# Kernel optimization log

Measured on AMD Instinct MI355X. Metric: run time of the kernel, lower is better.

## Reference

```python
import jax, jax.numpy as jnp
import numpy as np

H = 64  # hidden_size hardcoded in the module


def setup_inputs() -> dict:
    key = jax.random.key(0)
    ks = jax.random.split(key, 8)
    B, T, I, O = 4096, 256, 128, 10
    s_ih = 1.0 / np.sqrt(H)
    return {
        "x": jax.random.normal(ks[0], (B, T, I), dtype=jnp.float32),
        # PyTorch LSTM params, gate order (i, f, g, o)
        "W_ih": jax.random.uniform(ks[1], (4 * H, I), minval=-s_ih, maxval=s_ih, dtype=jnp.float32),
        "W_hh": jax.random.uniform(ks[2], (4 * H, H), minval=-s_ih, maxval=s_ih, dtype=jnp.float32),
        "b_ih": jax.random.uniform(ks[3], (4 * H,), minval=-s_ih, maxval=s_ih, dtype=jnp.float32),
        "b_hh": jax.random.uniform(ks[4], (4 * H,), minval=-s_ih, maxval=s_ih, dtype=jnp.float32),
        "W_out": jax.random.uniform(ks[5], (O, H), minval=-s_ih, maxval=s_ih, dtype=jnp.float32),
        "b_out": jax.random.uniform(ks[6], (O,), minval=-s_ih, maxval=s_ih, dtype=jnp.float32),
    }


def _lstm_last_h(x, W_ih, W_hh, b_ih, b_hh):
    B, T, I = x.shape
    # Precompute input contributions for all timesteps: [T, B, 4H]
    gx = jnp.einsum('bti,gi->tbg', x, W_ih) + (b_ih + b_hh)

    def step(carry, g_t):
        h, c = carry
        g = g_t + h @ W_hh.T  # [B, 4H]
        i = jax.nn.sigmoid(g[:, 0 * H:1 * H])
        f = jax.nn.sigmoid(g[:, 1 * H:2 * H])
        gg = jnp.tanh(g[:, 2 * H:3 * H])
        o = jax.nn.sigmoid(g[:, 3 * H:4 * H])
        c = f * c + i * gg
        h = o * jnp.tanh(c)
        return (h, c), None

    h0 = jnp.zeros((B, H), dtype=x.dtype)
    c0 = jnp.zeros((B, H), dtype=x.dtype)
    (h_last, _), _ = jax.lax.scan(step, (h0, c0), gx)
    return h_last


def reference(x, W_ih, W_hh, b_ih, b_hh, W_out, b_out):
    # forward reshapes x to [B, T, I]; our x is already that shape.
    h_last = _lstm_last_h(x, W_ih, W_hh, b_ih, b_hh)  # r_out[:, -1, :]
    return h_last @ W_out.T + b_out
```

## Files before the change

kernel.cpp:

```cpp
#include <hip/hip_runtime.h>


typedef __attribute__((ext_vector_type(8))) short bf16x8;
typedef __attribute__((ext_vector_type(4))) float f32x4;
typedef __attribute__((ext_vector_type(4))) int i32x4;

#define T_STEPS 256
#define L2E 1.44269504f

__device__ __forceinline__ short f2bf(float f) {
    unsigned u = __float_as_uint(f);
    u += 0x7FFFu + ((u >> 16) & 1u);
    return (short)(u >> 16);
}
__device__ __forceinline__ unsigned cvt_pk(float lo, float hi) {
    unsigned r;
    asm("v_cvt_pk_bf16_f32 %0, %1, %2" : "=v"(r) : "v"(lo), "v"(hi));
    return r;
}
__device__ __forceinline__ float frcp(float x) {
    float r; asm("v_rcp_f32 %0, %1" : "=v"(r) : "v"(x)); return r;
}
__device__ __forceinline__ float fexp2(float x) {
    float r; asm("v_exp_f32 %0, %1" : "=v"(r) : "v"(x)); return r;
}
__device__ __forceinline__ float sigm(float x) { return frcp(1.0f + fexp2(x * -L2E)); }
__device__ __forceinline__ float tanh_f(float x) { return 1.0f - 2.0f * frcp(1.0f + fexp2(x * (2.0f * L2E))); }

#define MF(A, Bf, C) (C) = __builtin_amdgcn_mfma_f32_16x16x32_bf16((A), (Bf), (C), 0, 0, 0)
#define PACK8(Av, Bv, W) { (W).x = cvt_pk((Av)[0], (Av)[1]); (W).y = cvt_pk((Av)[2], (Av)[3]); \
                           (W).z = cvt_pk((Bv)[0], (Bv)[1]); (W).w = cvt_pk((Bv)[2], (Bv)[3]); }

__global__ __launch_bounds__(256, 1) void lstm_fused_kernel(
    const float* __restrict__ x,
    const float* __restrict__ W_ih,
    const float* __restrict__ W_hh,
    const float* __restrict__ b_ih,
    const float* __restrict__ b_hh,
    const float* __restrict__ W_out,
    const float* __restrict__ b_out,
    float* __restrict__ out)
{
    __shared__ __align__(16) char smem[24576];

    const int tid  = threadIdx.x;
    const int lane = tid & 63;
    const int q    = tid >> 6;
    const int l15  = lane & 15;
    const int l4   = lane >> 4;
    const int b0   = blockIdx.x * 16;

    bf16x8 Bih[4][4];
    bf16x8 Bhh[4][2];
    f32x4  biasC[4];
#pragma unroll
    for (int nt = 0; nt < 4; ++nt) {
        const int row = nt * 64 + q * 16 + l15;
#pragma unroll
        for (int ks = 0; ks < 4; ++ks) {
            const float* p = W_ih + row * 128 + ks * 32 + l4 * 8;
            f32x4 a = *(const f32x4*)p;
            f32x4 b = *(const f32x4*)(p + 4);
            bf16x8 w;
#pragma unroll
            for (int j = 0; j < 4; ++j) { w[j] = f2bf(a[j]); w[4 + j] = f2bf(b[j]); }
            Bih[nt][ks] = w;
        }
#pragma unroll
        for (int ks = 0; ks < 2; ++ks) {
            const float* p = W_hh + row * 64 + ks * 32 + l4 * 8;
            f32x4 a = *(const f32x4*)p;
            f32x4 b = *(const f32x4*)(p + 4);
            bf16x8 w;
#pragma unroll
            for (int j = 0; j < 4; ++j) { w[j] = f2bf(a[j]); w[4 + j] = f2bf(b[j]); }
            Bhh[nt][ks] = w;
        }
        const float bb = b_ih[row] + b_hh[row];
        biasC[nt] = (f32x4){bb, bb, bb, bb};
    }

    const int sc  = tid & 15;
    const int sb  = tid >> 4;
    const int sks = sc >> 2;
    const int schunk = ((sc & 3) << 4) | sb;
    const int xf_wr  = (((sks * 64 + schunk) * 16) ^ ((sks & 3) << 6));
    const float* xrow = x + (size_t)(b0 + sb) * T_STEPS * 128 + sc * 8;

    int xf_rd[4];
#pragma unroll
    for (int ks = 0; ks < 4; ++ks)
        xf_rd[ks] = (((ks * 64 + lane) * 16) ^ ((ks & 3) << 6));

    int hb_wr[4];
#pragma unroll
    for (int r = 0; r < 4; ++r) {
        const int b = l4 * 4 + r;
        const int j = q * 16 + l15;
        hb_wr[r] = ((b * 128 + j * 2) ^ ((b & 7) << 4) ^ ((b >> 3) << 5));
    }
    int hb_rd[2];
#pragma unroll
    for (int ks = 0; ks < 2; ++ks)
        hb_rd[ks] = ((l15 * 128 + ks * 64 + l4 * 16) ^ ((l15 & 7) << 4) ^ ((l15 >> 3) << 5));

#pragma unroll
    for (int s = 0; s < 3; ++s) {
        f32x4 a = *(const f32x4*)(xrow + (size_t)s * 128);
        f32x4 b = *(const f32x4*)(xrow + (size_t)s * 128 + 4);
        i32x4 w; PACK8(a, b, w);
        *(i32x4*)(smem + s * 4096 + xf_wr) = w;
    }
    f32x4 P0_[4], P1_[4];
#pragma unroll
    for (int s = 0; s < 4; ++s) {
        P0_[s] = *(const f32x4*)(xrow + (size_t)(s + 3) * 128);
        P1_[s] = *(const f32x4*)(xrow + (size_t)(s + 3) * 128 + 4);
    }
    ((unsigned long long*)(smem + 16384 + 2048))[tid] = 0ull;

    asm volatile("s_waitcnt lgkmcnt(0)" ::: "memory");
    __builtin_amdgcn_s_barrier();

    float c[4]  = {0.f, 0.f, 0.f, 0.f};
    float hl[4] = {0.f, 0.f, 0.f, 0.f};

    f32x4 accA[4], accB[4];
    {
        bf16x8 Ax0 = *(const bf16x8*)(smem + xf_rd[0]);
        bf16x8 Ax1 = *(const bf16x8*)(smem + xf_rd[1]);
        bf16x8 Ax2 = *(const bf16x8*)(smem + xf_rd[2]);
        bf16x8 Ax3 = *(const bf16x8*)(smem + xf_rd[3]);
#pragma unroll
        for (int nt = 0; nt < 4; ++nt) accA[nt] = biasC[nt];
        MF(Ax0, Bih[0][0], accA[0]); MF(Ax0, Bih[1][0], accA[1]);
        MF(Ax0, Bih[2][0], accA[2]); MF(Ax0, Bih[3][0], accA[3]);
        MF(Ax1, Bih[0][1], accA[0]); MF(Ax1, Bih[1][1], accA[1]);
        MF(Ax1, Bih[2][1], accA[2]); MF(Ax1, Bih[3][1], accA[3]);
        MF(Ax2, Bih[0][2], accA[0]); MF(Ax2, Bih[1][2], accA[1]);
        MF(Ax2, Bih[2][2], accA[2]); MF(Ax2, Bih[3][2], accA[3]);
        MF(Ax3, Bih[0][3], accA[0]); MF(Ax3, Bih[1][3], accA[1]);
        MF(Ax3, Bih[2][3], accA[2]); MF(Ax3, Bih[3][3], accA[3]);
    }

#define WINDOW(tt, T4, ACUR, ANXT)                                             \
  {                                                                            \
    const char* hbR = smem + 16384 + ((((T4) & 1) ^ 1) * 2048);                \
    char*       hbW = smem + 16384 + (((T4) & 1) * 2048);                      \
    const char* xfb = smem + ((((T4) + 1) & 3) * 4096);                        \
    char*       xfw = smem + ((((T4) + 3) & 3) * 4096);                        \
    bf16x8 Ah0 = *(const bf16x8*)(hbR + hb_rd[0]);                             \
    bf16x8 Ah1 = *(const bf16x8*)(hbR + hb_rd[1]);                             \
    MF(Ah0, Bhh[0][0], ACUR[0]); MF(Ah0, Bhh[1][0], ACUR[1]);                  \
    MF(Ah0, Bhh[2][0], ACUR[2]); MF(Ah0, Bhh[3][0], ACUR[3]);                  \
    MF(Ah1, Bhh[0][1], ACUR[0]); MF(Ah1, Bhh[1][1], ACUR[1]);                  \
    MF(Ah1, Bhh[2][1], ACUR[2]); MF(Ah1, Bhh[3][1], ACUR[3]);                  \
    bf16x8 Ax0 = *(const bf16x8*)(xfb + xf_rd[0]);                             \
    bf16x8 Ax1 = *(const bf16x8*)(xfb + xf_rd[1]);                             \
    bf16x8 Ax2 = *(const bf16x8*)(xfb + xf_rd[2]);                             \
    bf16x8 Ax3 = *(const bf16x8*)(xfb + xf_rd[3]);                             \
    ANXT[0] = biasC[0]; ANXT[1] = biasC[1];                                    \
    ANXT[2] = biasC[2]; ANXT[3] = biasC[3];                                    \
    MF(Ax0, Bih[0][0], ANXT[0]); MF(Ax0, Bih[1][0], ANXT[1]);                  \
    MF(Ax0, Bih[2][0], ANXT[2]); MF(Ax0, Bih[3][0], ANXT[3]);                  \
    MF(Ax1, Bih[0][1], ANXT[0]); MF(Ax1, Bih[1][1], ANXT[1]);                  \
    MF(Ax1, Bih[2][1], ANXT[2]); MF(Ax1, Bih[3][1], ANXT[3]);                  \
    MF(Ax2, Bih[0][2], ANXT[0]); MF(Ax2, Bih[1][2], ANXT[1]);                  \
    MF(Ax2, Bih[2][2], ANXT[2]); MF(Ax2, Bih[3][2], ANXT[3]);                  \
    MF(Ax3, Bih[0][3], ANXT[0]); MF(Ax3, Bih[1][3], ANXT[1]);                  \
    MF(Ax3, Bih[2][3], ANXT[2]); MF(Ax3, Bih[3][3], ANXT[3]);                  \
    {                                                                          \
      i32x4 w; PACK8(P0_[(T4)], P1_[(T4)], w);                                 \
      *(i32x4*)(xfw + xf_wr) = w;                                              \
      int tc = (tt) + 7; tc = tc > 255 ? 255 : tc;                             \
      P0_[(T4)] = *(const f32x4*)(xrow + (size_t)tc * 128);                    \
      P1_[(T4)] = *(const f32x4*)(xrow + (size_t)tc * 128 + 4);                \
    }                                                                          \
    _Pragma("unroll")                                                          \
    for (int r = 0; r < 4; ++r) {                                              \
      float iv = sigm(ACUR[0][r]);                                             \
      float fv = sigm(ACUR[1][r]);                                             \
      float gv = tanh_f(ACUR[2][r]);                                           \
      float ov = sigm(ACUR[3][r]);                                             \
      float cc = fv * c[r] + iv * gv;                                          \
      c[r] = cc;                                                               \
      hl[r] = ov * tanh_f(cc);                                                 \
    }                                                                          \
    {                                                                          \
      unsigned w01 = cvt_pk(hl[0], hl[1]);                                     \
      unsigned w23 = cvt_pk(hl[2], hl[3]);                                     \
      *(short*)(hbW + hb_wr[0]) = (short)w01;                                  \
      *(short*)(hbW + hb_wr[1]) = (short)(w01 >> 16);                          \
      *(short*)(hbW + hb_wr[2]) = (short)w23;                                  \
      *(short*)(hbW + hb_wr[3]) = (short)(w23 >> 16);                          \
    }                                                                          \
    asm volatile("s_waitcnt lgkmcnt(0)" ::: "memory");                         \
    __builtin_amdgcn_s_barrier();                                              \
  }

    for (int t = 0; t < T_STEPS; t += 4) {
        WINDOW(t,     0, accA, accB);
        WINDOW(t + 1, 1, accB, accA);
        WINDOW(t + 2, 2, accA, accB);
        WINDOW(t + 3, 3, accB, accA);
    }
#undef WINDOW

#pragma unroll
    for (int r = 0; r < 4; ++r) {
        const int b = l4 * 4 + r;
        const int j = q * 16 + l15;
        *(float*)(smem + 20480 + (b * 64 + j) * 4) = hl[r];
    }
    asm volatile("s_waitcnt lgkmcnt(0)" ::: "memory");
    __builtin_amdgcn_s_barrier();

    if (tid < 160) {
        const int b = tid / 10;
        const int o = tid - b * 10;
        const f32x4* hf = (const f32x4*)(smem + 20480 + b * 256);
        const f32x4* wr = (const f32x4*)(W_out + o * 64);
        float s = b_out[o];
#pragma unroll
        for (int j4 = 0; j4 < 16; ++j4) {
            f32x4 h4 = hf[j4];
            f32x4 w4 = wr[j4];
            s += h4[0] * w4[0] + h4[1] * w4[1] + h4[2] * w4[2] + h4[3] * w4[3];
        }
        out[(b0 + b) * 10 + o] = s;
    }
}

extern "C" void kernel_launch(void* const* d_in, const int* in_sizes, int n_in,
                              void* d_out, int out_size, void* d_ws, size_t ws_size,
                              hipStream_t stream) {
    const float* x     = (const float*)d_in[0];
    const float* W_ih  = (const float*)d_in[1];
    const float* W_hh  = (const float*)d_in[2];
    const float* b_ih  = (const float*)d_in[3];
    const float* b_hh  = (const float*)d_in[4];
    const float* W_out = (const float*)d_in[5];
    const float* b_out = (const float*)d_in[6];
    (void)in_sizes; (void)n_in; (void)out_size; (void)d_ws; (void)ws_size;

    lstm_fused_kernel<<<dim3(256), dim3(256), 0, stream>>>(
        x, W_ih, W_hh, b_ih, b_hh, W_out, b_out, (float*)d_out);
}
```

Baseline: 177.8 us.

## Double waves per block, split gate nonlinearity across wave pairs

Raises the block from 256 to 512 threads. Each pair of waves computes the same MFMA gate tile redundantly, and each wave evaluates the nonlinearity for only two of the four rows, halving the serial transcendental work per wave on the recurrent critical path. The x staging is re-split so each thread loads one f32x4 instead of two. The cost is duplicated MFMA work, more register pressure under launch_bounds(512,2), and a barrier spanning twice as many waves.

```diff
diff --git a/kernel.cpp b/kernel.cpp
--- a/kernel.cpp
+++ b/kernel.cpp
@@ -3,10 +3,15 @@
 
 typedef __attribute__((ext_vector_type(8))) short bf16x8;
 typedef __attribute__((ext_vector_type(4))) float f32x4;
-typedef __attribute__((ext_vector_type(4))) int i32x4;
+typedef __attribute__((ext_vector_type(2))) unsigned u32x2;
 
 #define T_STEPS 256
 #define L2E 1.44269504f
+
+#define XF_OFF 0
+#define H_OFF  16384
+#define HF_OFF 20480
+#define LDS_SZ 24576
 
 __device__ __forceinline__ short f2bf(float f) {
     unsigned u = __float_as_uint(f);
@@ -18,20 +23,15 @@
     asm("v_cvt_pk_bf16_f32 %0, %1, %2" : "=v"(r) : "v"(lo), "v"(hi));
     return r;
 }
-__device__ __forceinline__ float frcp(float x) {
-    float r; asm("v_rcp_f32 %0, %1" : "=v"(r) : "v"(x)); return r;
-}
-__device__ __forceinline__ float fexp2(float x) {
-    float r; asm("v_exp_f32 %0, %1" : "=v"(r) : "v"(x)); return r;
-}
+__device__ __forceinline__ float frcp(float x) { float r; asm("v_rcp_f32 %0, %1" : "=v"(r) : "v"(x)); return r; }
+__device__ __forceinline__ float fexp2(float x) { float r; asm("v_exp_f32 %0, %1" : "=v"(r) : "v"(x)); return r; }
 __device__ __forceinline__ float sigm(float x) { return frcp(1.0f + fexp2(x * -L2E)); }
 __device__ __forceinline__ float tanh_f(float x) { return 1.0f - 2.0f * frcp(1.0f + fexp2(x * (2.0f * L2E))); }
 
 #define MF(A, Bf, C) (C) = __builtin_amdgcn_mfma_f32_16x16x32_bf16((A), (Bf), (C), 0, 0, 0)
-#define PACK8(Av, Bv, W) { (W).x = cvt_pk((Av)[0], (Av)[1]); (W).y = cvt_pk((Av)[2], (Av)[3]); \
-                           (W).z = cvt_pk((Bv)[0], (Bv)[1]); (W).w = cvt_pk((Bv)[2], (Bv)[3]); }
-
-__global__ __launch_bounds__(256, 1) void lstm_fused_kernel(
+#define SYNC { asm volatile("s_waitcnt lgkmcnt(0)" ::: "memory"); __builtin_amdgcn_s_barrier(); }
+
+__global__ __launch_bounds__(512, 2) void lstm_kernel(
     const float* __restrict__ x,
     const float* __restrict__ W_ih,
     const float* __restrict__ W_hh,
@@ -41,11 +41,13 @@
     const float* __restrict__ b_out,
     float* __restrict__ out)
 {
-    __shared__ __align__(16) char smem[24576];
+    __shared__ __align__(16) char smem[LDS_SZ];
 
     const int tid  = threadIdx.x;
     const int lane = tid & 63;
-    const int q    = tid >> 6;
+    const int w    = tid >> 6;
+    const int m    = w >> 1;
+    const int e    = w & 1;
     const int l15  = lane & 15;
     const int l4   = lane >> 4;
     const int b0   = blockIdx.x * 16;
@@ -55,82 +57,80 @@
     f32x4  biasC[4];
 #pragma unroll
     for (int nt = 0; nt < 4; ++nt) {
-        const int row = nt * 64 + q * 16 + l15;
+        const int row = nt * 64 + m * 16 + l15;
 #pragma unroll
         for (int ks = 0; ks < 4; ++ks) {
             const float* p = W_ih + row * 128 + ks * 32 + l4 * 8;
             f32x4 a = *(const f32x4*)p;
             f32x4 b = *(const f32x4*)(p + 4);
-            bf16x8 w;
-#pragma unroll
-            for (int j = 0; j < 4; ++j) { w[j] = f2bf(a[j]); w[4 + j] = f2bf(b[j]); }
-            Bih[nt][ks] = w;
+            bf16x8 wv;
+#pragma unroll
+            for (int j = 0; j < 4; ++j) { wv[j] = f2bf(a[j]); wv[4 + j] = f2bf(b[j]); }
+            Bih[nt][ks] = wv;
         }
 #pragma unroll
         for (int ks = 0; ks < 2; ++ks) {
             const float* p = W_hh + row * 64 + ks * 32 + l4 * 8;
             f32x4 a = *(const f32x4*)p;
             f32x4 b = *(const f32x4*)(p + 4);
-            bf16x8 w;
-#pragma unroll
-            for (int j = 0; j < 4; ++j) { w[j] = f2bf(a[j]); w[4 + j] = f2bf(b[j]); }
-            Bhh[nt][ks] = w;
+            bf16x8 wv;
+#pragma unroll
+            for (int j = 0; j < 4; ++j) { wv[j] = f2bf(a[j]); wv[4 + j] = f2bf(b[j]); }
+            Bhh[nt][ks] = wv;
         }
         const float bb = b_ih[row] + b_hh[row];
         biasC[nt] = (f32x4){bb, bb, bb, bb};
     }
 
-    const int sc  = tid & 15;
-    const int sb  = tid >> 4;
-    const int sks = sc >> 2;
-    const int schunk = ((sc & 3) << 4) | sb;
-    const int xf_wr  = (((sks * 64 + schunk) * 16) ^ ((sks & 3) << 6));
-    const float* xrow = x + (size_t)(b0 + sb) * T_STEPS * 128 + sc * 8;
-
     int xf_rd[4];
 #pragma unroll
     for (int ks = 0; ks < 4; ++ks)
         xf_rd[ks] = (((ks * 64 + lane) * 16) ^ ((ks & 3) << 6));
 
-    int hb_wr[4];
-#pragma unroll
-    for (int r = 0; r < 4; ++r) {
-        const int b = l4 * 4 + r;
-        const int j = q * 16 + l15;
-        hb_wr[r] = ((b * 128 + j * 2) ^ ((b & 7) << 4) ^ ((b >> 3) << 5));
+    const int jcol = m * 16 + l15;
+    int hb_wr[2];
+#pragma unroll
+    for (int u = 0; u < 2; ++u) {
+        const int b = l4 * 4 + 2 * e + u;
+        hb_wr[u] = ((b * 128 + jcol * 2) ^ ((b & 7) << 4) ^ ((b >> 3) << 5));
     }
     int hb_rd[2];
 #pragma unroll
     for (int ks = 0; ks < 2; ++ks)
         hb_rd[ks] = ((l15 * 128 + ks * 64 + l4 * 16) ^ ((l15 & 7) << 4) ^ ((l15 >> 3) << 5));
 
+    const int srow = tid >> 5;
+    const int scc  = tid & 31;
+    const int sks  = scc >> 3;
+    const int sl4  = (scc & 7) >> 1;
+    const int sh   = scc & 1;
+    const int xf_wr = (((sks * 64 + sl4 * 16 + srow) * 16 + sh * 8) ^ ((sks & 3) << 6));
+    const float* xsrc = x + (size_t)(b0 + srow) * (T_STEPS * 128) + scc * 4;
+
 #pragma unroll
     for (int s = 0; s < 3; ++s) {
-        f32x4 a = *(const f32x4*)(xrow + (size_t)s * 128);
-        f32x4 b = *(const f32x4*)(xrow + (size_t)s * 128 + 4);
-        i32x4 w; PACK8(a, b, w);
-        *(i32x4*)(smem + s * 4096 + xf_wr) = w;
-    }
-    f32x4 P0_[4], P1_[4];
-#pragma unroll
-    for (int s = 0; s < 4; ++s) {
-        P0_[s] = *(const f32x4*)(xrow + (size_t)(s + 3) * 128);
-        P1_[s] = *(const f32x4*)(xrow + (size_t)(s + 3) * 128 + 4);
-    }
-    ((unsigned long long*)(smem + 16384 + 2048))[tid] = 0ull;
-
-    asm volatile("s_waitcnt lgkmcnt(0)" ::: "memory");
-    __builtin_amdgcn_s_barrier();
-
-    float c[4]  = {0.f, 0.f, 0.f, 0.f};
-    float hl[4] = {0.f, 0.f, 0.f, 0.f};
+        f32x4 v = *(const f32x4*)(xsrc + (size_t)s * 128);
+        u32x2 wv; wv.x = cvt_pk(v[0], v[1]); wv.y = cvt_pk(v[2], v[3]);
+        *(u32x2*)(smem + XF_OFF + s * 4096 + xf_wr) = wv;
+    }
+    f32x4 P[4];
+#pragma unroll
+    for (int s = 0; s < 4; ++s)
+        P[s] = *(const f32x4*)(xsrc + (size_t)(s + 3) * 128);
+
+    ((unsigned*)(smem + H_OFF + 2048))[tid] = 0u;
+
+    SYNC;
+
+    float c[2]  = {0.f, 0.f};
+    float hl[2] = {0.f, 0.f};
 
     f32x4 accA[4], accB[4];
     {
-        bf16x8 Ax0 = *(const bf16x8*)(smem + xf_rd[0]);
-        bf16x8 Ax1 = *(const bf16x8*)(smem + xf_rd[1]);
-        bf16x8 Ax2 = *(const bf16x8*)(smem + xf_rd[2]);
-        bf16x8 Ax3 = *(const bf16x8*)(smem + xf_rd[3]);
+        bf16x8 Ax0 = *(const bf16x8*)(smem + XF_OFF + xf_rd[0]);
+        bf16x8 Ax1 = *(const bf16x8*)(smem + XF_OFF + xf_rd[1]);
+        bf16x8 Ax2 = *(const bf16x8*)(smem + XF_OFF + xf_rd[2]);
+        bf16x8 Ax3 = *(const bf16x8*)(smem + XF_OFF + xf_rd[3]);
 #pragma unroll
         for (int nt = 0; nt < 4; ++nt) accA[nt] = biasC[nt];
         MF(Ax0, Bih[0][0], accA[0]); MF(Ax0, Bih[1][0], accA[1]);
@@ -143,12 +143,32 @@
         MF(Ax3, Bih[2][3], accA[2]); MF(Ax3, Bih[3][3], accA[3]);
     }
 
+#define NONLIN(ACUR, R0, R1, hbW)                                              \
+    {                                                                          \
+      float iv0 = sigm(ACUR[0][R0]);                                           \
+      float fv0 = sigm(ACUR[1][R0]);                                           \
+      float gv0 = tanh_f(ACUR[2][R0]);                                         \
+      float ov0 = sigm(ACUR[3][R0]);                                           \
+      float iv1 = sigm(ACUR[0][R1]);                                           \
+      float fv1 = sigm(ACUR[1][R1]);                                           \
+      float gv1 = tanh_f(ACUR[2][R1]);                                         \
+      float ov1 = sigm(ACUR[3][R1]);                                           \
+      float cc0 = fv0 * c[0] + iv0 * gv0;                                      \
+      float cc1 = fv1 * c[1] + iv1 * gv1;                                      \
+      c[0] = cc0; c[1] = cc1;                                                  \
+      hl[0] = ov0 * tanh_f(cc0);                                               \
+      hl[1] = ov1 * tanh_f(cc1);                                               \
+      unsigned wp = cvt_pk(hl[0], hl[1]);                                      \
+      *(short*)((hbW) + hb_wr[0]) = (short)wp;                                 \
+      *(short*)((hbW) + hb_wr[1]) = (short)(wp >> 16);                         \
+    }
+
 #define WINDOW(tt, T4, ACUR, ANXT)                                             \
   {                                                                            \
-    const char* hbR = smem + 16384 + ((((T4) & 1) ^ 1) * 2048);                \
-    char*       hbW = smem + 16384 + (((T4) & 1) * 2048);                      \
-    const char* xfb = smem + ((((T4) + 1) & 3) * 4096);                        \
-    char*       xfw = smem + ((((T4) + 3) & 3) * 4096);                        \
+    const char* hbR = smem + H_OFF + ((((T4) & 1) ^ 1) * 2048);                \
+    char*       hbW = smem + H_OFF + (((T4) & 1) * 2048);                      \
+    const char* xfb = smem + XF_OFF + ((((T4) + 1) & 3) * 4096);               \
+    char*       xfw = smem + XF_OFF + ((((T4) + 3) & 3) * 4096);               \
     bf16x8 Ah0 = *(const bf16x8*)(hbR + hb_rd[0]);                             \
     bf16x8 Ah1 = *(const bf16x8*)(hbR + hb_rd[1]);                             \
     MF(Ah0, Bhh[0][0], ACUR[0]); MF(Ah0, Bhh[1][0], ACUR[1]);                  \
@@ -170,32 +190,14 @@
     MF(Ax3, Bih[0][3], ANXT[0]); MF(Ax3, Bih[1][3], ANXT[1]);                  \
     MF(Ax3, Bih[2][3], ANXT[2]); MF(Ax3, Bih[3][3], ANXT[3]);                  \
     {                                                                          \
-      i32x4 w; PACK8(P0_[(T4)], P1_[(T4)], w);                                 \
-      *(i32x4*)(xfw + xf_wr) = w;                                              \
+      u32x2 wv; wv.x = cvt_pk(P[(T4)][0], P[(T4)][1]);                         \
+      wv.y = cvt_pk(P[(T4)][2], P[(T4)][3]);                                   \
+      *(u32x2*)(xfw + xf_wr) = wv;                                             \
       int tc = (tt) + 7; tc = tc > 255 ? 255 : tc;                             \
-      P0_[(T4)] = *(const f32x4*)(xrow + (size_t)tc * 128);                    \
-      P1_[(T4)] = *(const f32x4*)(xrow + (size_t)tc * 128 + 4);                \
+      P[(T4)] = *(const f32x4*)(xsrc + (size_t)tc * 128);                      \
     }                                                                          \
-    _Pragma("unroll")                                                          \
-    for (int r = 0; r < 4; ++r) {                                              \
-      float iv = sigm(ACUR[0][r]);                                             \
-      float fv = sigm(ACUR[1][r]);                                             \
-      float gv = tanh_f(ACUR[2][r]);                                           \
-      float ov = sigm(ACUR[3][r]);                                             \
-      float cc = fv * c[r] + iv * gv;                                          \
-      c[r] = cc;                                                               \
-      hl[r] = ov * tanh_f(cc);                                                 \
-    }                                                                          \
-    {                                                                          \
-      unsigned w01 = cvt_pk(hl[0], hl[1]);                                     \
-      unsigned w23 = cvt_pk(hl[2], hl[3]);                                     \
-      *(short*)(hbW + hb_wr[0]) = (short)w01;                                  \
-      *(short*)(hbW + hb_wr[1]) = (short)(w01 >> 16);                          \
-      *(short*)(hbW + hb_wr[2]) = (short)w23;                                  \
-      *(short*)(hbW + hb_wr[3]) = (short)(w23 >> 16);                          \
-    }                                                                          \
-    asm volatile("s_waitcnt lgkmcnt(0)" ::: "memory");                         \
-    __builtin_amdgcn_s_barrier();                                              \
+    if (e == 0) { NONLIN(ACUR, 0, 1, hbW) } else { NONLIN(ACUR, 2, 3, hbW) }   \
+    SYNC;                                                                      \
   }
 
     for (int t = 0; t < T_STEPS; t += 4) {
@@ -205,20 +207,19 @@
         WINDOW(t + 3, 3, accB, accA);
     }
 #undef WINDOW
-
-#pragma unroll
-    for (int r = 0; r < 4; ++r) {
-        const int b = l4 * 4 + r;
-        const int j = q * 16 + l15;
-        *(float*)(smem + 20480 + (b * 64 + j) * 4) = hl[r];
-    }
-    asm volatile("s_waitcnt lgkmcnt(0)" ::: "memory");
-    __builtin_amdgcn_s_barrier();
+#undef NONLIN
+
+#pragma unroll
+    for (int u = 0; u < 2; ++u) {
+        const int b = l4 * 4 + 2 * e + u;
+        *(float*)(smem + HF_OFF + (b * 64 + jcol) * 4) = hl[u];
+    }
+    SYNC;
 
     if (tid < 160) {
         const int b = tid / 10;
         const int o = tid - b * 10;
-        const f32x4* hf = (const f32x4*)(smem + 20480 + b * 256);
+        const f32x4* hf = (const f32x4*)(smem + HF_OFF + b * 256);
         const f32x4* wr = (const f32x4*)(W_out + o * 64);
         float s = b_out[o];
 #pragma unroll
@@ -243,6 +244,6 @@
     const float* b_out = (const float*)d_in[6];
     (void)in_sizes; (void)n_in; (void)out_size; (void)d_ws; (void)ws_size;
 
-    lstm_fused_kernel<<<dim3(256), dim3(256), 0, stream>>>(
+    lstm_kernel<<<dim3(256), dim3(512), 0, stream>>>(
         x, W_ih, W_hh, b_ih, b_hh, W_out, b_out, (float*)d_out);
 }
```

After: 216.6 us. 21.8% more time.
